# Performance work log

Hardware: AMD Instinct MI355X
Metric: run time of the kernel (lower is better)

The kernel has to match this reference:

```python
import jax, jax.numpy as jnp
import numpy as np

N, E, F_IN, D, K, OUT = 50000, 800000, 16, 64, 3, 3


def _safe_dinv(deg):
    safe = jnp.where(deg > 0, deg, 1.0)
    return jnp.where(deg > 0, jax.lax.rsqrt(safe), 0.0)


def _gcn(x, src, dst, W, b, n):
    # GCNConv(improved=True): A_hat = A + 2I, sym normalization
    xw = x @ W
    ones = jnp.ones(src.shape[0], x.dtype)
    deg = jax.ops.segment_sum(ones, dst, num_segments=n) + 2.0  # self-loop weight 2
    dinv = jax.lax.rsqrt(deg)  # deg >= 2, always finite
    agg = jax.ops.segment_sum((dinv[src] * dinv[dst])[:, None] * xw[src], dst, num_segments=n)
    agg = agg + (2.0 * dinv * dinv)[:, None] * xw  # self-loop contribution
    return agg + b


def _cheb(x, src, dst, dinv, W, b, n):
    # ChebConv, normalization='sym', lambda_max=2.0  =>  L_hat = -D^{-1/2} A D^{-1/2}
    coef = (dinv[src] * dinv[dst])[:, None]

    def lhat(z):
        return -jax.ops.segment_sum(coef * z[src], dst, num_segments=n)

    z_prev = x
    out = x @ W[0]
    z_cur = lhat(x)
    out = out + z_cur @ W[1]
    for k in range(2, W.shape[0]):
        z_next = 2.0 * lhat(z_cur) - z_prev
        out = out + z_next @ W[k]
        z_prev, z_cur = z_cur, z_next
    return out + b


def _gclstm(x, H, C, src, dst, dinv, wx, bx, wh, bh, wc, bg, n):
    # gate order in stacks: [i, f, c, o]; peephole wc: [i, f, o]
    gx = lambda g: _cheb(x, src, dst, dinv, wx[g], bx[g], n)
    gh = lambda g: _cheb(H, src, dst, dinv, wh[g], bh[g], n)
    i = jax.nn.sigmoid(gx(0) + gh(0) + wc[0] * C + bg[0])
    f = jax.nn.sigmoid(gx(1) + gh(1) + wc[1] * C + bg[1])
    t = jnp.tanh(gx(2) + gh(2) + bg[2])
    Cn = f * C + i * t
    o = jax.nn.sigmoid(gx(3) + gh(3) + wc[2] * Cn + bg[3])
    return o * jnp.tanh(Cn), Cn


def _forward(x, edge_index, p):
    (w_gcn1, b_gcn1, w_gcn2, b_gcn2,
     wx1, bx1, wh1, bh1, wc1, bg1,
     wx2, bx2, wh2, bh2, wc2, bg2,
     wx3, bx3, wh3, bh3, wc3, bg3,
     lin_w, lin_b) = p
    src, dst = edge_index[0], edge_index[1]
    n = x.shape[0]
    ones = jnp.ones(src.shape[0], x.dtype)
    deg_c = jax.ops.segment_sum(ones, dst, num_segments=n)  # Cheb: no self loops
    dinv_c = _safe_dinv(deg_c)

    h = jax.nn.relu(_gcn(x, src, dst, w_gcn1, b_gcn1, n))
    h = jax.nn.relu(_gcn(h, src, dst, w_gcn2, b_gcn2, n))

    z = jnp.zeros((n, wh1.shape[-1]), h.dtype)  # H=C=None -> zeros per cell
    H1, _ = _gclstm(h, z, z, src, dst, dinv_c, wx1, bx1, wh1, bh1, wc1, bg1, n)
    H2, _ = _gclstm(H1, z, z, src, dst, dinv_c, wx2, bx2, wh2, bh2, wc2, bg2, n)
    H3, _ = _gclstm(H2, z, z, src, dst, dinv_c, wx3, bx3, wh3, bh3, wc3, bg3, n)
    return jax.nn.relu(H3) @ lin_w + lin_b


def setup_inputs() -> dict:
    key = jax.random.key(0)

    def nrm(i, shape):
        return 0.1 * jax.random.normal(jax.random.fold_in(key, i), shape, jnp.float32)

    inp = {}
    inp["x"] = jax.random.normal(jax.random.fold_in(key, 0), (N, F_IN), jnp.float32)
    inp["edge_index"] = jax.random.randint(jax.random.fold_in(key, 1), (2, E), 0, N)
    inp["w_gcn1"] = nrm(2, (F_IN, D))
    inp["b_gcn1"] = nrm(3, (D,))
    inp["w_gcn2"] = nrm(4, (D, D))
    inp["b_gcn2"] = nrm(5, (D,))
    i = 6
    for l in (1, 2, 3):
        inp[f"wx{l}"] = nrm(i, (4, K, D, D)); i += 1
        inp[f"bx{l}"] = nrm(i, (4, D)); i += 1
        inp[f"wh{l}"] = nrm(i, (4, K, D, D)); i += 1
        inp[f"bh{l}"] = nrm(i, (4, D)); i += 1
        inp[f"wc{l}"] = nrm(i, (3, D)); i += 1
        inp[f"bg{l}"] = nrm(i, (4, D)); i += 1
    inp["lin_w"] = nrm(i, (D, OUT))
    inp["lin_b"] = nrm(i + 1, (OUT,))
    return inp


def reference(x, edge_index, w_gcn1, b_gcn1, w_gcn2, b_gcn2,
              wx1, bx1, wh1, bh1, wc1, bg1,
              wx2, bx2, wh2, bh2, wc2, bg2,
              wx3, bx3, wh3, bh3, wc3, bg3,
              lin_w, lin_b):
    p = (w_gcn1, b_gcn1, w_gcn2, b_gcn2,
         wx1, bx1, wh1, bh1, wc1, bg1,
         wx2, bx2, wh2, bh2, wc2, bg2,
         wx3, bx3, wh3, bh3, wc3, bg3,
         lin_w, lin_b)
    return _forward(x, edge_index, p)
```

## Files before the change

### kernel.cpp

```cpp
#include <hip/hip_runtime.h>


typedef _Float16 half8 __attribute__((ext_vector_type(8)));
typedef float f32x4 __attribute__((ext_vector_type(4)));

__global__ void count_deg_x_kernel(const int* __restrict__ ei, int* __restrict__ deg,
                                   int E, int chunk) {
  int range = blockIdx.x & 7;
  int lo = range * chunk, hi = lo + chunk;
  int stride = (gridDim.x >> 3) * blockDim.x;
  for (int e = (blockIdx.x >> 3) * blockDim.x + threadIdx.x; e < E; e += stride) {
    int d = ei[E + e];
    if (d >= lo && d < hi) atomicAdd(&deg[d], 1);
  }
}

__global__ void fill_x_kernel(const int* __restrict__ ei, int* __restrict__ cursor,
                              unsigned short* __restrict__ csr, int E, int chunk) {
  int range = blockIdx.x & 7;
  int lo = range * chunk, hi = lo + chunk;
  int stride = (gridDim.x >> 3) * blockDim.x;
  for (int e = (blockIdx.x >> 3) * blockDim.x + threadIdx.x; e < E; e += stride) {
    int d = ei[E + e];
    if (d >= lo && d < hi) {
      int pos = atomicAdd(&cursor[d], 1);
      csr[pos] = (unsigned short)ei[e];
    }
  }
}

__global__ void scan_block_sums(const int* __restrict__ deg, int* __restrict__ bsum, int n) {
  int tid = threadIdx.x;
  int i = blockIdx.x * 256 + tid;
  int v = (i < n) ? deg[i] : 0;
  for (int off = 32; off; off >>= 1) v += __shfl_down(v, off);
  __shared__ int ws[4];
  int lane = tid & 63, wid = tid >> 6;
  if (lane == 0) ws[wid] = v;
  __syncthreads();
  if (tid == 0) bsum[blockIdx.x] = ws[0] + ws[1] + ws[2] + ws[3];
}

__global__ void scan_final(const int* __restrict__ deg, const int* __restrict__ bsum, int nb,
                           int* __restrict__ rowptr, int* __restrict__ cursor,
                           float* __restrict__ dg, float* __restrict__ dc,
                           float* __restrict__ rc, int n) {
  __shared__ int tmp[256];
  __shared__ int ws[4];
  __shared__ int base_sh;
  int tid = threadIdx.x;
  int v0 = (tid < nb && tid < (int)blockIdx.x) ? bsum[tid] : 0;
  for (int off = 32; off; off >>= 1) v0 += __shfl_down(v0, off);
  if ((tid & 63) == 0) ws[tid >> 6] = v0;
  __syncthreads();
  if (tid == 0) base_sh = ws[0] + ws[1] + ws[2] + ws[3];
  int i = blockIdx.x * 256 + tid;
  int v = (i < n) ? deg[i] : 0;
  tmp[tid] = v;
  __syncthreads();
  for (int off = 1; off < 256; off <<= 1) {
    int t = (tid >= off) ? tmp[tid - off] : 0;
    __syncthreads();
    tmp[tid] += t;
    __syncthreads();
  }
  if (i < n) {
    int excl = tmp[tid] - v + base_sh;
    rowptr[i] = excl;
    cursor[i] = excl;
    dg[i] = rsqrtf((float)v + 2.f);
    dc[i] = (v > 0) ? rsqrtf((float)v) : 0.f;
    rc[i] = (v > 0) ? sqrtf((float)v) : 0.f;
  }
}

__global__ void cast_x16_kernel(const float* __restrict__ x, const float* __restrict__ dg,
                                _Float16* __restrict__ x16s, int total) {
  int i = blockIdx.x * blockDim.x + threadIdx.x;
  if (i < total) x16s[i] = (_Float16)(dg[i >> 4] * x[i]);
}

__global__ void pack_all_kernel(const float* __restrict__ wx0, const float* __restrict__ wx1,
                                const float* __restrict__ wx2, const float* __restrict__ Wg2,
                                _Float16* __restrict__ Wpk, _Float16* __restrict__ Wpk2) {
  int idx = blockIdx.x * 256 + threadIdx.x;
  if (idx < 3 * 3 * 192 * 64) {
    int l = idx / 36864;
    int r = idx % 36864;
    int g = r / 12288;
    int r2 = r % 12288;
    int k = r2 / 64;
    int n = r2 % 64;
    const float* wx = (l == 0) ? wx0 : (l == 1 ? wx1 : wx2);
    int gs = (g == 0) ? 0 : (g == 1 ? 2 : 3);
    int tau = k >> 6, kd = k & 63;
    size_t base = ((size_t)gs * 3) * 4096 + (size_t)kd * 64 + n;
    float v;
    if (tau == 0)      v = wx[base] - wx[base + 2 * 4096];
    else if (tau == 1) v = wx[base + 1 * 4096];
    else               v = 2.f * wx[base + 2 * 4096];
    int kc = k >> 5, klo = k & 31;
    int lane = ((klo >> 3) << 4) | (n & 15);
    int j = klo & 7;
    int nt = n >> 4;
    Wpk[((((size_t)l * 3 + g) * 6 + kc) * 4 + nt) * 512 + (size_t)lane * 8 + j] = (_Float16)v;
  } else if (idx < 3 * 3 * 192 * 64 + 4096) {
    int i2 = idx - 110592;
    int k = i2 >> 6, n = i2 & 63;
    float v = Wg2[k * 64 + n];
    int kc = k >> 5, klo = k & 31;
    int lane = ((klo >> 3) << 4) | (n & 15);
    int j = klo & 7;
    int nt = n >> 4;
    Wpk2[(((size_t)kc * 4 + nt) * 64 + lane) * 8 + j] = (_Float16)v;
  }
}

__global__ __launch_bounds__(256) void gcn1_fused_kernel(
    const _Float16* __restrict__ X16s, const float* __restrict__ W1,
    const float* __restrict__ b1, const float* __restrict__ dg,
    _Float16* __restrict__ OUTs,
    const int* __restrict__ rowptr, const int* __restrict__ deg,
    const unsigned short* __restrict__ csr, int n) {
  __shared__ float w1s[16 * 64];
  int tid = threadIdx.x;
  for (int i = tid; i < 1024; i += 256) w1s[i] = W1[i];
  __syncthreads();
  int node = blockIdx.x * 8 + (tid >> 5);
  if (node >= n) return;
  int lane = tid & 63;
  int l32 = tid & 31;
  int eg = l32 >> 1, c8 = l32 & 1;
  int beg = rowptr[node], end = beg + deg[node];
  const half8* IN8 = (const half8*)X16s;
  float acc[8];
#pragma unroll
  for (int j = 0; j < 8; ++j) acc[j] = 0.f;
  for (int p = beg + eg; p < end; p += 16) {
    int s = csr[p];
    half8 v = IN8[(size_t)s * 2 + c8];
#pragma unroll
    for (int j = 0; j < 8; ++j) acc[j] += (float)v[j];
  }
#pragma unroll
  for (int j = 0; j < 8; ++j) {
    acc[j] += __shfl_xor(acc[j], 2);
    acc[j] += __shfl_xor(acc[j], 4);
    acc[j] += __shfl_xor(acc[j], 8);
    acc[j] += __shfl_xor(acc[j], 16);
  }
  float dt = dg[node];
  half8 self = IN8[(size_t)node * 2 + c8];
  float v8[8];
#pragma unroll
  for (int j = 0; j < 8; ++j) v8[j] = dt * acc[j] + 2.f * dt * (float)self[j];
  float agg[16];
  int base = lane & 32;
#pragma unroll
  for (int k = 0; k < 16; ++k) agg[k] = __shfl(v8[k & 7], base + (k >> 3));
  float h0 = b1[l32], h1 = b1[l32 + 32];
#pragma unroll
  for (int k = 0; k < 16; ++k) {
    h0 += agg[k] * w1s[k * 64 + l32];
    h1 += agg[k] * w1s[k * 64 + l32 + 32];
  }
  OUTs[(size_t)node * 64 + l32]      = (_Float16)(dt * fmaxf(h0, 0.f));
  OUTs[(size_t)node * 64 + l32 + 32] = (_Float16)(dt * fmaxf(h1, 0.f));
}

template <int MODE>
__global__ void gather_kernel(const int* __restrict__ rowptr, const int* __restrict__ deg,
                              const unsigned short* __restrict__ csr,
                              const float* __restrict__ dinv,
                              const _Float16* __restrict__ INs,
                              _Float16* __restrict__ OUT, int n) {
  int node = blockIdx.x * (blockDim.x >> 6) + (threadIdx.x >> 6);
  if (node >= n) return;
  int lane = threadIdx.x & 63;
  int eg = lane >> 3, c8 = lane & 7;
  int beg = rowptr[node], end = beg + deg[node];
  const half8* IN8 = (const half8*)INs;
  float acc[8], acc2[8];
#pragma unroll
  for (int j = 0; j < 8; ++j) { acc[j] = 0.f; acc2[j] = 0.f; }
  int p = beg + eg;
  for (; p + 8 < end; p += 16) {
    int s0 = csr[p];
    int s1 = csr[p + 8];
    half8 v0 = IN8[(size_t)s0 * 8 + c8];
    half8 v1 = IN8[(size_t)s1 * 8 + c8];
#pragma unroll
    for (int j = 0; j < 8; ++j) { acc[j] += (float)v0[j]; acc2[j] += (float)v1[j]; }
  }
  if (p < end) {
    int s = csr[p];
    half8 v = IN8[(size_t)s * 8 + c8];
#pragma unroll
    for (int j = 0; j < 8; ++j) acc[j] += (float)v[j];
  }
#pragma unroll
  for (int j = 0; j < 8; ++j) {
    acc[j] += acc2[j];
    acc[j] += __shfl_xor(acc[j], 8);
    acc[j] += __shfl_xor(acc[j], 16);
    acc[j] += __shfl_xor(acc[j], 32);
  }
  if (eg == 0) {
    float dt = dinv[node];
    size_t o8 = (size_t)node * 8 + c8;
    half8 r;
    if (MODE == 0) {
      half8 self = IN8[o8];
#pragma unroll
      for (int j = 0; j < 8; ++j) r[j] = (_Float16)(dt * acc[j] + 2.f * dt * (float)self[j]);
    } else if (MODE == 1) {
      float s = -dt * dt;
#pragma unroll
      for (int j = 0; j < 8; ++j) r[j] = (_Float16)(s * acc[j]);
    } else {
#pragma unroll
      for (int j = 0; j < 8; ++j) r[j] = (_Float16)(-dt * acc[j]);
    }
    ((half8*)OUT)[o8] = r;
  }
}

__global__ __launch_bounds__(256) void gcn2_mfma_kernel(
    const _Float16* __restrict__ A, const _Float16* __restrict__ W2,
    const float* __restrict__ bias, const float* __restrict__ dc,
    _Float16* __restrict__ OUT, _Float16* __restrict__ OUTs, int n) {
  int tid = threadIdx.x;
  int wid = tid >> 6, lane = tid & 63;
  int n0 = blockIdx.x * 64;
  int row = n0 + wid * 16 + (lane & 15);
  int rowc = min(row, n - 1);
  int ksub = (lane >> 4) << 3;
  int dbase = lane & 15;
  const _Float16* Wlane = W2 + (size_t)lane * 8;
  f32x4 acc[4];
#pragma unroll
  for (int nt = 0; nt < 4; ++nt) {
    float b = bias[nt * 16 + dbase];
    acc[nt] = (f32x4){b, b, b, b};
  }
#pragma unroll
  for (int kc = 0; kc < 2; ++kc) {
    half8 a = *(const half8*)&A[(size_t)rowc * 64 + (kc << 5) + ksub];
#pragma unroll
    for (int nt = 0; nt < 4; ++nt) {
      half8 b = *(const half8*)(Wlane + (size_t)(kc * 4 + nt) * 512);
      acc[nt] = __builtin_amdgcn_mfma_f32_16x16x32_f16(a, b, acc[nt], 0, 0, 0);
    }
  }
  int mrow = n0 + wid * 16 + ((lane >> 4) << 2);
#pragma unroll
  for (int nt = 0; nt < 4; ++nt) {
    int d = nt * 16 + dbase;
#pragma unroll
    for (int r = 0; r < 4; ++r) {
      int node = mrow + r;
      if (node < n) {
        float h = fmaxf(acc[nt][r], 0.f);
        OUT[(size_t)node * 64 + d] = (_Float16)h;
        OUTs[(size_t)node * 64 + d] = (_Float16)(dc[node] * h);
      }
    }
  }
}

template <int FINAL>
__global__ __launch_bounds__(256) void gate_mfma_kernel(
    const _Float16* __restrict__ X, const _Float16* __restrict__ Z1s,
    const _Float16* __restrict__ Y,
    const _Float16* __restrict__ Wl,
    const float* __restrict__ bx, const float* __restrict__ bh, const float* __restrict__ bg,
    const float* __restrict__ wc, const float* __restrict__ dc,
    const float* __restrict__ rinv,
    _Float16* __restrict__ H, _Float16* __restrict__ Hs,
    const float* __restrict__ lw, const float* __restrict__ lb,
    float* __restrict__ out, int n) {
  int tid = threadIdx.x;
  int wid = tid >> 6, lane = tid & 63;
  int n0 = blockIdx.x * 64;
  int row = n0 + wid * 16 + (lane & 15);
  int rowc = min(row, n - 1);
  int ksub = (lane >> 4) << 3;
  const _Float16* Wlane = Wl + (size_t)lane * 8;
  int dbase = lane & 15;
  float rv = rinv[rowc];

  f32x4 acc[3][4];
#pragma unroll
  for (int g = 0; g < 3; ++g) {
    int gs = (g == 0) ? 0 : (g == 1 ? 2 : 3);
#pragma unroll
    for (int nt = 0; nt < 4; ++nt) {
      int d = nt * 16 + dbase;
      float b = bx[gs * 64 + d] + bh[gs * 64 + d] + bg[gs * 64 + d];
      acc[g][nt] = (f32x4){b, b, b, b};
    }
  }
  const _Float16* T[3] = {X, Z1s, Y};
#pragma unroll
  for (int kc = 0; kc < 6; ++kc) {
    const _Float16* t = T[kc >> 1];
    half8 a = *(const half8*)&t[(size_t)rowc * 64 + ((kc & 1) << 5) + ksub];
    if (kc >= 2 && kc < 4) {
#pragma unroll
      for (int j = 0; j < 8; ++j) a[j] = (_Float16)((float)a[j] * rv);
    }
#pragma unroll
    for (int g = 0; g < 3; ++g) {
#pragma unroll
      for (int nt = 0; nt < 4; ++nt) {
        half8 b = *(const half8*)(Wlane + (size_t)((g * 6 + kc) * 4 + nt) * 512);
        acc[g][nt] = __builtin_amdgcn_mfma_f32_16x16x32_f16(a, b, acc[g][nt], 0, 0, 0);
      }
    }
  }
  int mrow = n0 + wid * 16 + ((lane >> 4) << 2);
  float po[4][3];
  if (FINAL) {
#pragma unroll
    for (int r = 0; r < 4; ++r) { po[r][0] = 0.f; po[r][1] = 0.f; po[r][2] = 0.f; }
  }
#pragma unroll
  for (int nt = 0; nt < 4; ++nt) {
    int d = nt * 16 + dbase;
    float wcd = wc[128 + d];
#pragma unroll
    for (int r = 0; r < 4; ++r) {
      float ig = 1.f / (1.f + expf(-acc[0][nt][r]));
      float tt = tanhf(acc[1][nt][r]);
      float Cn = ig * tt;
      float og = 1.f / (1.f + expf(-(acc[2][nt][r] + wcd * Cn)));
      float h = og * tanhf(Cn);
      if (FINAL) {
        float rl = fmaxf(h, 0.f);
        po[r][0] += rl * lw[d * 3 + 0];
        po[r][1] += rl * lw[d * 3 + 1];
        po[r][2] += rl * lw[d * 3 + 2];
      } else {
        int node = mrow + r;
        if (node < n) {
          H[(size_t)node * 64 + d] = (_Float16)h;
          Hs[(size_t)node * 64 + d] = (_Float16)(dc[node] * h);
        }
      }
    }
  }
  if (FINAL) {
#pragma unroll
    for (int m = 1; m < 16; m <<= 1) {
#pragma unroll
      for (int r = 0; r < 4; ++r) {
        po[r][0] += __shfl_xor(po[r][0], m);
        po[r][1] += __shfl_xor(po[r][1], m);
        po[r][2] += __shfl_xor(po[r][2], m);
      }
    }
    if (dbase == 0) {
#pragma unroll
      for (int r = 0; r < 4; ++r) {
        int node = mrow + r;
        if (node < n) {
          out[(size_t)node * 3 + 0] = po[r][0] + lb[0];
          out[(size_t)node * 3 + 1] = po[r][1] + lb[1];
          out[(size_t)node * 3 + 2] = po[r][2] + lb[2];
        }
      }
    }
  }
}

extern "C" void kernel_launch(void* const* d_in, const int* in_sizes, int n_in,
                              void* d_out, int out_size, void* d_ws, size_t ws_size,
                              hipStream_t stream) {
  const float* x      = (const float*)d_in[0];
  const int*   ei     = (const int*)d_in[1];
  const float* w_gcn1 = (const float*)d_in[2];
  const float* b_gcn1 = (const float*)d_in[3];
  const float* w_gcn2 = (const float*)d_in[4];
  const float* b_gcn2 = (const float*)d_in[5];
  const float* wx[3]  = {(const float*)d_in[6],  (const float*)d_in[12], (const float*)d_in[18]};
  const float* bx[3]  = {(const float*)d_in[7],  (const float*)d_in[13], (const float*)d_in[19]};
  const float* bh[3]  = {(const float*)d_in[9],  (const float*)d_in[15], (const float*)d_in[21]};
  const float* wc[3]  = {(const float*)d_in[10], (const float*)d_in[16], (const float*)d_in[22]};
  const float* bg[3]  = {(const float*)d_in[11], (const float*)d_in[17], (const float*)d_in[23]};
  const float* lin_w  = (const float*)d_in[24];
  const float* lin_b  = (const float*)d_in[25];
  float* out = (float*)d_out;

  int N = in_sizes[0] / 16;
  int E = in_sizes[1] / 2;
  int nsb = (N + 255) / 256;
  int chunk = (N + 7) / 8;

  char* ws = (char*)d_ws;
  size_t off = 0;
  auto alloc = [&](size_t bytes) {
    void* p = ws + off;
    off = (off + bytes + 255) & ~(size_t)255;
    return p;
  };
  int* deg        = (int*)alloc((size_t)N * 4);
  int* rowptr     = (int*)alloc((size_t)N * 4);
  int* cursor     = (int*)alloc((size_t)N * 4);
  int* bsum       = (int*)alloc((size_t)nsb * 4);
  unsigned short* csr = (unsigned short*)alloc((size_t)E * 2);
  float* dinv_g   = (float*)alloc((size_t)N * 4);
  float* dinv_c   = (float*)alloc((size_t)N * 4);
  float* rinv_c   = (float*)alloc((size_t)N * 4);
  _Float16* Wpk   = (_Float16*)alloc((size_t)3 * 36864 * 2);
  _Float16* Wpk2  = (_Float16*)alloc((size_t)4096 * 2);
  _Float16* x16s  = (_Float16*)alloc((size_t)N * 16 * 2);
  _Float16* bufA  = (_Float16*)alloc((size_t)N * 64 * 2);
  _Float16* bufAs = (_Float16*)alloc((size_t)N * 64 * 2);
  _Float16* bufB  = (_Float16*)alloc((size_t)N * 64 * 2);
  _Float16* bufC  = (_Float16*)alloc((size_t)N * 64 * 2);
  (void)ws_size; (void)n_in; (void)out_size;

  hipMemsetAsync(deg, 0, (size_t)N * 4, stream);
  count_deg_x_kernel<<<4096, 256, 0, stream>>>(ei, deg, E, chunk);
  scan_block_sums<<<nsb, 256, 0, stream>>>(deg, bsum, N);
  scan_final<<<nsb, 256, 0, stream>>>(deg, bsum, nsb, rowptr, cursor,
                                      dinv_g, dinv_c, rinv_c, N);
  fill_x_kernel<<<4096, 256, 0, stream>>>(ei, cursor, csr, E, chunk);
  pack_all_kernel<<<(114688 + 255) / 256, 256, 0, stream>>>(wx[0], wx[1], wx[2], w_gcn2,
                                                            Wpk, Wpk2);
  cast_x16_kernel<<<(N * 16 + 255) / 256, 256, 0, stream>>>(x, dinv_g, x16s, N * 16);

  int nb64 = (N + 63) / 64;
  int nbw  = (N + 3) / 4;
  int nb8  = (N + 7) / 8;

  gcn1_fused_kernel<<<nb8, 256, 0, stream>>>(x16s, w_gcn1, b_gcn1, dinv_g, bufB,
                                             rowptr, deg, csr, N);
  gather_kernel<0><<<nbw, 256, 0, stream>>>(rowptr, deg, csr, dinv_g, bufB, bufC, N);
  gcn2_mfma_kernel<<<nb64, 256, 0, stream>>>(bufC, Wpk2, b_gcn2, dinv_c, bufA, bufAs, N);

  for (int l = 0; l < 3; ++l) {
    gather_kernel<1><<<nbw, 256, 0, stream>>>(rowptr, deg, csr, dinv_c, bufAs, bufB, N);
    gather_kernel<3><<<nbw, 256, 0, stream>>>(rowptr, deg, csr, dinv_c, bufB, bufC, N);
    if (l < 2) {
      gate_mfma_kernel<0><<<nb64, 256, 0, stream>>>(bufA, bufB, bufC, Wpk + (size_t)l * 36864,
                                                    bx[l], bh[l], bg[l], wc[l], dinv_c, rinv_c,
                                                    bufA, bufAs, nullptr, nullptr, nullptr, N);
    } else {
      gate_mfma_kernel<1><<<nb64, 256, 0, stream>>>(bufA, bufB, bufC, Wpk + (size_t)l * 36864,
                                                    bx[l], bh[l], bg[l], wc[l], dinv_c, rinv_c,
                                                    nullptr, nullptr, lin_w, lin_b, out, N);
    }
  }
}
```

Measured before the change: 357.8 us.

## Merge setup kernels and preload CSR indices via wave shuffles in gathers

The deg memset is folded into the weight-packing kernel, and the x cast is folded into the block-sum kernel, where the degree normalisation is recomputed inline. Together these drop several small launches from the setup chain. In the gather and gcn1 kernels, each lane loads one neighbour index up front with a coalesced read and broadcasts it via __shfl, instead of reading csr indices serially inside the loop. High-degree nodes fall back to a strided loop for the remaining edges. The cost is extra predication and shuffle work per edge.

```diff
diff --git a/kernel.cpp b/kernel.cpp
--- a/kernel.cpp
+++ b/kernel.cpp
@@ -29,16 +29,62 @@
   }
 }
 
-__global__ void scan_block_sums(const int* __restrict__ deg, int* __restrict__ bsum, int n) {
+__global__ void prep_kernel(const float* __restrict__ wx0, const float* __restrict__ wx1,
+                            const float* __restrict__ wx2, const float* __restrict__ Wg2,
+                            _Float16* __restrict__ Wpk, _Float16* __restrict__ Wpk2,
+                            int* __restrict__ deg, int n) {
+  int idx = blockIdx.x * 256 + threadIdx.x;
+  if (idx < 110592) {
+    int l = idx / 36864;
+    int r = idx % 36864;
+    int g = r / 12288;
+    int r2 = r % 12288;
+    int k = r2 / 64;
+    int nn = r2 % 64;
+    const float* wx = (l == 0) ? wx0 : (l == 1 ? wx1 : wx2);
+    int gs = (g == 0) ? 0 : (g == 1 ? 2 : 3);
+    int tau = k >> 6, kd = k & 63;
+    size_t base = ((size_t)gs * 3) * 4096 + (size_t)kd * 64 + nn;
+    float v;
+    if (tau == 0)      v = wx[base] - wx[base + 2 * 4096];
+    else if (tau == 1) v = wx[base + 1 * 4096];
+    else               v = 2.f * wx[base + 2 * 4096];
+    int kc = k >> 5, klo = k & 31;
+    int lane = ((klo >> 3) << 4) | (nn & 15);
+    int j = klo & 7;
+    int nt = nn >> 4;
+    Wpk[((((size_t)l * 3 + g) * 6 + kc) * 4 + nt) * 512 + (size_t)lane * 8 + j] = (_Float16)v;
+  } else if (idx < 114688) {
+    int i2 = idx - 110592;
+    int k = i2 >> 6, nn = i2 & 63;
+    float v = Wg2[k * 64 + nn];
+    int kc = k >> 5, klo = k & 31;
+    int lane = ((klo >> 3) << 4) | (nn & 15);
+    int j = klo & 7;
+    int nt = nn >> 4;
+    Wpk2[(((size_t)kc * 4 + nt) * 64 + lane) * 8 + j] = (_Float16)v;
+  } else if (idx < 114688 + n) {
+    deg[idx - 114688] = 0;
+  }
+}
+
+__global__ void sums_cast_kernel(const int* __restrict__ deg, int* __restrict__ bsum, int nsb,
+                                 const float* __restrict__ x, _Float16* __restrict__ x16s,
+                                 int n) {
   int tid = threadIdx.x;
-  int i = blockIdx.x * 256 + tid;
-  int v = (i < n) ? deg[i] : 0;
-  for (int off = 32; off; off >>= 1) v += __shfl_down(v, off);
-  __shared__ int ws[4];
-  int lane = tid & 63, wid = tid >> 6;
-  if (lane == 0) ws[wid] = v;
-  __syncthreads();
-  if (tid == 0) bsum[blockIdx.x] = ws[0] + ws[1] + ws[2] + ws[3];
+  if ((int)blockIdx.x < nsb) {
+    int i = blockIdx.x * 256 + tid;
+    int v = (i < n) ? deg[i] : 0;
+    for (int off = 32; off; off >>= 1) v += __shfl_down(v, off);
+    __shared__ int ws[4];
+    int lane = tid & 63, wid = tid >> 6;
+    if (lane == 0) ws[wid] = v;
+    __syncthreads();
+    if (tid == 0) bsum[blockIdx.x] = ws[0] + ws[1] + ws[2] + ws[3];
+  } else {
+    int i = (blockIdx.x - nsb) * 256 + tid;
+    if (i < n * 16) x16s[i] = (_Float16)(rsqrtf((float)deg[i >> 4] + 2.f) * x[i]);
+  }
 }
 
 __global__ void scan_final(const int* __restrict__ deg, const int* __restrict__ bsum, int nb,
@@ -74,48 +120,6 @@
   }
 }
 
-__global__ void cast_x16_kernel(const float* __restrict__ x, const float* __restrict__ dg,
-                                _Float16* __restrict__ x16s, int total) {
-  int i = blockIdx.x * blockDim.x + threadIdx.x;
-  if (i < total) x16s[i] = (_Float16)(dg[i >> 4] * x[i]);
-}
-
-__global__ void pack_all_kernel(const float* __restrict__ wx0, const float* __restrict__ wx1,
-                                const float* __restrict__ wx2, const float* __restrict__ Wg2,
-                                _Float16* __restrict__ Wpk, _Float16* __restrict__ Wpk2) {
-  int idx = blockIdx.x * 256 + threadIdx.x;
-  if (idx < 3 * 3 * 192 * 64) {
-    int l = idx / 36864;
-    int r = idx % 36864;
-    int g = r / 12288;
-    int r2 = r % 12288;
-    int k = r2 / 64;
-    int n = r2 % 64;
-    const float* wx = (l == 0) ? wx0 : (l == 1 ? wx1 : wx2);
-    int gs = (g == 0) ? 0 : (g == 1 ? 2 : 3);
-    int tau = k >> 6, kd = k & 63;
-    size_t base = ((size_t)gs * 3) * 4096 + (size_t)kd * 64 + n;
-    float v;
-    if (tau == 0)      v = wx[base] - wx[base + 2 * 4096];
-    else if (tau == 1) v = wx[base + 1 * 4096];
-    else               v = 2.f * wx[base + 2 * 4096];
-    int kc = k >> 5, klo = k & 31;
-    int lane = ((klo >> 3) << 4) | (n & 15);
-    int j = klo & 7;
-    int nt = n >> 4;
-    Wpk[((((size_t)l * 3 + g) * 6 + kc) * 4 + nt) * 512 + (size_t)lane * 8 + j] = (_Float16)v;
-  } else if (idx < 3 * 3 * 192 * 64 + 4096) {
-    int i2 = idx - 110592;
-    int k = i2 >> 6, n = i2 & 63;
-    float v = Wg2[k * 64 + n];
-    int kc = k >> 5, klo = k & 31;
-    int lane = ((klo >> 3) << 4) | (n & 15);
-    int j = klo & 7;
-    int nt = n >> 4;
-    Wpk2[(((size_t)kc * 4 + nt) * 64 + lane) * 8 + j] = (_Float16)v;
-  }
-}
-
 __global__ __launch_bounds__(256) void gcn1_fused_kernel(
     const _Float16* __restrict__ X16s, const float* __restrict__ W1,
     const float* __restrict__ b1, const float* __restrict__ dg,
@@ -131,12 +135,23 @@
   int lane = tid & 63;
   int l32 = tid & 31;
   int eg = l32 >> 1, c8 = l32 & 1;
-  int beg = rowptr[node], end = beg + deg[node];
+  int beg = rowptr[node], dgg = deg[node];
   const half8* IN8 = (const half8*)X16s;
+  int idx = 0;
+  if (l32 < dgg) idx = csr[beg + l32];
   float acc[8];
 #pragma unroll
   for (int j = 0; j < 8; ++j) acc[j] = 0.f;
-  for (int p = beg + eg; p < end; p += 16) {
+  int kmaxU = (dgg + 15) >> 4; if (kmaxU > 2) kmaxU = 2;
+  for (int k = 0; k < kmaxU; ++k) {
+    int s = __shfl(idx, eg + 16 * k, 32);
+    half8 v = IN8[(size_t)s * 2 + c8];
+    if (eg + 16 * k < dgg) {
+#pragma unroll
+      for (int j = 0; j < 8; ++j) acc[j] += (float)v[j];
+    }
+  }
+  for (int p = beg + eg + 32; p < beg + dgg; p += 16) {
     int s = csr[p];
     half8 v = IN8[(size_t)s * 2 + c8];
 #pragma unroll
@@ -178,21 +193,38 @@
   if (node >= n) return;
   int lane = threadIdx.x & 63;
   int eg = lane >> 3, c8 = lane & 7;
-  int beg = rowptr[node], end = beg + deg[node];
+  int beg = rowptr[node], dgg = deg[node];
   const half8* IN8 = (const half8*)INs;
+  int idx = 0;
+  if (lane < dgg) idx = csr[beg + lane];
   float acc[8], acc2[8];
 #pragma unroll
   for (int j = 0; j < 8; ++j) { acc[j] = 0.f; acc2[j] = 0.f; }
-  int p = beg + eg;
-  for (; p + 8 < end; p += 16) {
-    int s0 = csr[p];
-    int s1 = csr[p + 8];
+  int kmaxU = (dgg + 7) >> 3; if (kmaxU > 8) kmaxU = 8;
+  int k = 0;
+  for (; k + 2 <= kmaxU; k += 2) {
+    int s0 = __shfl(idx, eg + 8 * k);
+    int s1 = __shfl(idx, eg + 8 * k + 8);
     half8 v0 = IN8[(size_t)s0 * 8 + c8];
     half8 v1 = IN8[(size_t)s1 * 8 + c8];
-#pragma unroll
-    for (int j = 0; j < 8; ++j) { acc[j] += (float)v0[j]; acc2[j] += (float)v1[j]; }
-  }
-  if (p < end) {
+    if (eg + 8 * k < dgg) {
+#pragma unroll
+      for (int j = 0; j < 8; ++j) acc[j] += (float)v0[j];
+    }
+    if (eg + 8 * k + 8 < dgg) {
+#pragma unroll
+      for (int j = 0; j < 8; ++j) acc2[j] += (float)v1[j];
+    }
+  }
+  if (k < kmaxU) {
+    int s = __shfl(idx, eg + 8 * k);
+    half8 v = IN8[(size_t)s * 8 + c8];
+    if (eg + 8 * k < dgg) {
+#pragma unroll
+      for (int j = 0; j < 8; ++j) acc[j] += (float)v[j];
+    }
+  }
+  for (int p = beg + eg + 64; p < beg + dgg; p += 8) {
     int s = csr[p];
     half8 v = IN8[(size_t)s * 8 + c8];
 #pragma unroll
@@ -420,15 +452,13 @@
   _Float16* bufC  = (_Float16*)alloc((size_t)N * 64 * 2);
   (void)ws_size; (void)n_in; (void)out_size;
 
-  hipMemsetAsync(deg, 0, (size_t)N * 4, stream);
+  prep_kernel<<<(114688 + N + 255) / 256, 256, 0, stream>>>(wx[0], wx[1], wx[2], w_gcn2,
+                                                            Wpk, Wpk2, deg, N);
   count_deg_x_kernel<<<4096, 256, 0, stream>>>(ei, deg, E, chunk);
-  scan_block_sums<<<nsb, 256, 0, stream>>>(deg, bsum, N);
+  sums_cast_kernel<<<nsb + (N * 16 + 255) / 256, 256, 0, stream>>>(deg, bsum, nsb, x, x16s, N);
   scan_final<<<nsb, 256, 0, stream>>>(deg, bsum, nsb, rowptr, cursor,
                                       dinv_g, dinv_c, rinv_c, N);
   fill_x_kernel<<<4096, 256, 0, stream>>>(ei, cursor, csr, E, chunk);
-  pack_all_kernel<<<(114688 + 255) / 256, 256, 0, stream>>>(wx[0], wx[1], wx[2], w_gcn2,
-                                                            Wpk, Wpk2);
-  cast_x16_kernel<<<(N * 16 + 255) / 256, 256, 0, stream>>>(x, dinv_g, x16s, N * 16);
 
   int nb64 = (N + 63) / 64;
   int nbw  = (N + 3) / 4;
```

Result: faster. 345.3 us (-3.5%).
